# Optimization experiments

Hardware: AMD Instinct MI355X
Metric: run time of the kernel (lower is better)

Reference implementation:

```python
import jax, jax.numpy as jnp
import numpy as np

DIM = 512
NUM_HEADS = 8
HEAD_DIM = DIM // NUM_HEADS
SCALE = HEAD_DIM ** -0.5
B, T = 8, 1024


def setup_inputs() -> dict:
    key = jax.random.key(0)
    ks = jax.random.split(key, 6)
    x = jax.random.normal(ks[0], (B, T, DIM), dtype=jnp.float32)
    attn_mask = jax.random.randint(ks[1], (B, T, T), 0, 2) == 1  # bool [B,T,T]
    s = 1.0 / np.sqrt(DIM)
    qkv_w = jax.random.uniform(ks[2], (3 * DIM, DIM), jnp.float32, -s, s)
    qkv_b = jax.random.uniform(ks[3], (3 * DIM,), jnp.float32, -s, s)
    proj_w = jax.random.uniform(ks[4], (DIM, DIM), jnp.float32, -s, s)
    proj_b = jax.random.uniform(ks[5], (DIM,), jnp.float32, -s, s)
    return {"x": x, "attn_mask": attn_mask, "qkv_w": qkv_w, "qkv_b": qkv_b,
            "proj_w": proj_w, "proj_b": proj_b}


def reference(x, attn_mask, qkv_w, qkv_b, proj_w, proj_b):
    b, t, c = x.shape
    # QKV projection (torch Linear: x @ W.T + b), split into q,k,v heads
    qkv = x @ qkv_w.T + qkv_b                      # [b,t,3*c]
    qkv = qkv.reshape(b, t, 3, NUM_HEADS, HEAD_DIM)
    qkv = jnp.transpose(qkv, (2, 0, 3, 1, 4))      # [3,b,h,t,d]
    q, k, v = qkv[0], qkv[1], qkv[2]
    scores = jnp.einsum('bhqd,bhkd->bhqk', q, k) * SCALE  # [b,h,t,t]
    min_val = jnp.finfo(scores.dtype).min
    scores = jnp.where(attn_mask[:, None, :, :], min_val, scores)
    attn = jax.nn.softmax(scores, axis=-1)
    out = jnp.einsum('bhqk,bhkd->bhqd', attn, v)   # [b,h,t,d]
    out = jnp.transpose(out, (0, 2, 1, 3)).reshape(b, t, c)
    return out @ proj_w.T + proj_b
```

## Files before the change

kernel.cpp:

```cpp
#include <hip/hip_runtime.h>
#include <math.h>

#define DIM   512
#define NH    8
#define HD    64
#define BATCH 8
#define SEQ   1024
#define QSCALE 0.18033688011112042f

typedef unsigned short u16;
typedef unsigned int   u32;
typedef unsigned long long u64;
typedef __bf16 bf16x8 __attribute__((ext_vector_type(8)));
typedef float  f32x4  __attribute__((ext_vector_type(4)));

__device__ inline u16 f2bf(float f) {
  u32 u = __builtin_bit_cast(u32, f);
  return (u16)((u + 0x7fffu + ((u >> 16) & 1u)) >> 16);
}
__device__ inline float bf2f(u16 h) {
  return __builtin_bit_cast(float, (u32)h << 16);
}
__device__ inline u32 pk2(float a, float b) {
  return (u32)f2bf(a) | ((u32)f2bf(b) << 16);
}

__device__ inline void a16(const u16* g, u16* l) {
  __builtin_amdgcn_global_load_lds(
      (const __attribute__((address_space(1))) u32*)g,
      (__attribute__((address_space(3))) u32*)l, 16, 0, 0);
}


__device__ inline void decomp_body(const float* __restrict__ src, u16* ph,
                                   u16* pl, int t) {
  #pragma unroll
  for (int c = 0; c < 4; ++c) {
    const int cid = c * 256 + t;
    const int row = cid & 15, kc = cid >> 4;
    float f[8];
    *(float4*)&f[0] = *(const float4*)&src[row * DIM + kc * 8];
    *(float4*)&f[4] = *(const float4*)&src[row * DIM + kc * 8 + 4];
    u16 hv[8], lv[8];
    #pragma unroll
    for (int j = 0; j < 8; ++j) {
      hv[j] = f2bf(f[j]);
      lv[j] = f2bf(f[j] - bf2f(hv[j]));
    }
    *(uint4*)&ph[(size_t)cid * 8] = *(const uint4*)hv;
    *(uint4*)&pl[(size_t)cid * 8] = *(const uint4*)lv;
  }
}

__global__ __launch_bounds__(256) void prep(
    const int* __restrict__ mask, u64* __restrict__ bits,
    const float* __restrict__ x, u16* __restrict__ xhi, u16* __restrict__ xlo,
    const float* __restrict__ qkvw, u16* __restrict__ wqh, u16* __restrict__ wql,
    const float* __restrict__ projw, u16* __restrict__ wph, u16* __restrict__ wpl) {
  const int blk = blockIdx.x;
  const int t = threadIdx.x;
  if (blk < 32768) {
    const size_t gid = (size_t)blk * 256 + t;
    const int lane = t & 63;
    const size_t w = gid >> 6;
    const int v = mask[w * 64 + lane];
    const u64 b = __ballot(v != 0);
    if (lane == 0) {
      const int bb = (int)(w >> 14), q = (int)((w >> 4) & 1023),
                kt = (int)(w & 15);
      bits[(((size_t)(bb << 4 | kt)) << 10) | q] = b;
    }
  } else if (blk < 33280) {
    const int rg = blk - 32768;
    decomp_body(x + (size_t)rg * 16 * DIM, xhi + (size_t)rg * 8192,
                xlo + (size_t)rg * 8192, t);
  } else if (blk < 33376) {
    const int rg = blk - 33280;
    decomp_body(qkvw + (size_t)rg * 16 * DIM, wqh + (size_t)rg * 8192,
                wql + (size_t)rg * 8192, t);
  } else {
    const int rg = blk - 33376;
    decomp_body(projw + (size_t)rg * 16 * DIM, wph + (size_t)rg * 8192,
                wpl + (size_t)rg * 8192, t);
  }
}

template <bool QKV>
__global__ __launch_bounds__(256) void mfma_gemm(
    const u16* __restrict__ Agh, const u16* __restrict__ Agl,
    const u16* __restrict__ Bgh, const u16* __restrict__ Bgl,
    const float* __restrict__ bias, void* __restrict__ out0,
    u16* __restrict__ kfr, u16* __restrict__ vfr) {
  __shared__ u16 sAh[2][4096];
  __shared__ u16 sAl[2][4096];
  __shared__ u16 sBh[2][4096];
  __shared__ u16 sBl[2][4096];

  const int tid = threadIdx.x;
  const int lane = tid & 63;
  const int wv = tid >> 6;
  const int lk = lane & 15, lq = lane >> 4;
  const int m0 = blockIdx.x * 128, n0 = blockIdx.y * 128;
  const int wm = (wv & 1) * 4;
  const int wn = (wv >> 1) * 4;

  const u16* gAh = Agh + (size_t)(m0 >> 4) * 8192 + lane * 8;
  const u16* gAl = Agl + (size_t)(m0 >> 4) * 8192 + lane * 8;
  const u16* gBh = Bgh + (size_t)(n0 >> 4) * 8192 + lane * 8;
  const u16* gBl = Bgl + (size_t)(n0 >> 4) * 8192 + lane * 8;

  auto stage = [&](int bufi, int ki) {
    #pragma unroll
    for (int it = 0; it < 2; ++it) {
      const int t = it * 4 + wv;
      const size_t go = (size_t)t * 8192 + (size_t)ki * 512;
      const int lo_ = t * 512 + lane * 8;
      a16(gAh + go, &sAh[bufi][lo_]);
      a16(gAl + go, &sAl[bufi][lo_]);
      a16(gBh + go, &sBh[bufi][lo_]);
      a16(gBl + go, &sBl[bufi][lo_]);
    }
  };

  f32x4 acc[4][4];
  #pragma unroll
  for (int i = 0; i < 4; ++i)
    #pragma unroll
    for (int j = 0; j < 4; ++j) acc[i][j] = (f32x4){0.f, 0.f, 0.f, 0.f};

  stage(0, 0);
  __syncthreads();

  #pragma unroll 1
  for (int ki = 0; ki < 16; ++ki) {
    const int cur = ki & 1;
    bf16x8 ah[4], al[4], bh[4], bl[4];
    #pragma unroll
    for (int i = 0; i < 4; ++i) {
      ah[i] = *(const bf16x8*)&sAh[cur][(wm + i) * 512 + lane * 8];
      al[i] = *(const bf16x8*)&sAl[cur][(wm + i) * 512 + lane * 8];
      bh[i] = *(const bf16x8*)&sBh[cur][(wn + i) * 512 + lane * 8];
      bl[i] = *(const bf16x8*)&sBl[cur][(wn + i) * 512 + lane * 8];
    }
    if (ki < 15) stage(cur ^ 1, ki + 1);
    __builtin_amdgcn_sched_barrier(0);

    __builtin_amdgcn_s_setprio(1);
    #pragma unroll
    for (int i = 0; i < 4; ++i)
      #pragma unroll
      for (int j = 0; j < 4; ++j) {
        acc[i][j] = __builtin_amdgcn_mfma_f32_16x16x32_bf16(ah[i], bh[j], acc[i][j], 0, 0, 0);
        acc[i][j] = __builtin_amdgcn_mfma_f32_16x16x32_bf16(ah[i], bl[j], acc[i][j], 0, 0, 0);
        acc[i][j] = __builtin_amdgcn_mfma_f32_16x16x32_bf16(al[i], bh[j], acc[i][j], 0, 0, 0);
      }
    __builtin_amdgcn_s_setprio(0);

    __syncthreads();
  }

  #pragma unroll
  for (int j = 0; j < 4; ++j) {
    const int n = n0 + (wn + j) * 16 + lk;
    const float bv_ = bias[n];
    #pragma unroll
    for (int i = 0; i < 4; ++i) {
      const int mb = m0 + (wm + i) * 16 + lq * 4;
      if (QKV) {
        const int which = n >> 9, h = (n >> 6) & 7, d = n & 63;
        const int b = mb >> 10, tok0 = mb & 1023;
        const size_t hb = (size_t)((b << 3) + h) << 16;
        if (which == 2) {
          const size_t base = hb + ((size_t)(tok0 >> 6) << 12) +
                              ((size_t)((d >> 4) & 3) << 10) +
                              ((size_t)((tok0 >> 5) & 1) << 9) +
                              ((size_t)((d & 15) + (((tok0 >> 3) & 3) << 4)) << 3) +
                              (size_t)(tok0 & 7);
          uint2 o2;
          o2.x = pk2(acc[i][j][0] + bv_, acc[i][j][1] + bv_);
          o2.y = pk2(acc[i][j][2] + bv_, acc[i][j][3] + bv_);
          *(uint2*)&vfr[base] = o2;
        } else if (which == 1) {
          const size_t base = hb + ((size_t)(tok0 >> 4) << 10) +
                              ((size_t)(d >> 5) << 9) + (size_t)(d & 7) +
                              ((size_t)(((d >> 3) & 3) << 4) << 3);
          #pragma unroll
          for (int r = 0; r < 4; ++r)
            kfr[base + (((tok0 & 15) + r) << 3)] = f2bf(acc[i][j][r] + bv_);
        } else {
          u16* dst = (u16*)out0;
          #pragma unroll
          for (int r = 0; r < 4; ++r)
            dst[(((size_t)((b << 3) + h) << 10 | (tok0 + r)) << 6) + d] =
                f2bf((acc[i][j][r] + bv_) * QSCALE);
        }
      } else {
        #pragma unroll
        for (int r = 0; r < 4; ++r)
          ((float*)out0)[(size_t)(mb + r) * DIM + n] = acc[i][j][r] + bv_;
      }
    }
  }
}

__global__ __launch_bounds__(256) void attn_mfma(
    const u16* __restrict__ qg, const u16* __restrict__ kfr,
    const u16* __restrict__ vfr, const u64* __restrict__ bitsT,
    u16* __restrict__ ohi, u16* __restrict__ olo) {
  __shared__ u16 Kls[2][4096];
  __shared__ u16 Vls[2][4096];
  __shared__ u16 Ps[64 * 72];

  const int tid = threadIdx.x;
  const int lane = tid & 63;
  const int wv = tid >> 6;
  const int lk = lane & 15, lq = lane >> 4;
  const int bh = blockIdx.x;
  const int q0 = blockIdx.y * 64;
  const int bb = bh >> 3;
  const int q = q0 + wv * 16 + lk;

  const u16* qrow = qg + ((size_t)(bh << 10 | q) << 6);
  const bf16x8 bq0 = *(const bf16x8*)(qrow + lq * 8);
  const bf16x8 bq1 = *(const bf16x8*)(qrow + 32 + lq * 8);

  const u16* kh = kfr + ((size_t)bh << 16);
  const u16* vh = vfr + ((size_t)bh << 16);
  const u64* bitp = bitsT + ((size_t)bb << 14) + q;
  u16* pw = &Ps[(wv * 16 + lk) * 72];

  auto stage = [&](int bufi, int kt) {
    #pragma unroll
    for (int it = 0; it < 2; ++it) {
      const int c = it * 4 + wv;
      const int off = c * 512 + lane * 8;
      a16(kh + ((size_t)kt << 12) + off, &Kls[bufi][off]);
      a16(vh + ((size_t)kt << 12) + off, &Vls[bufi][off]);
    }
  };

  f32x4 o_[4];
  float l = 0.f;
  #pragma unroll
  for (int t = 0; t < 4; ++t) o_[t] = (f32x4){0.f, 0.f, 0.f, 0.f};

  stage(0, 0);
  __syncthreads();

  #pragma unroll 1
  for (int kt = 0; kt < 16; ++kt) {
    const int cur = kt & 1;
    const u64 wd = bitp[(size_t)kt << 10];

    bf16x8 ak0[4], ak1[4], vb0[4], vb1[4];
    #pragma unroll
    for (int t = 0; t < 4; ++t) {
      ak0[t] = *(const bf16x8*)&Kls[cur][t * 1024 + lane * 8];
      ak1[t] = *(const bf16x8*)&Kls[cur][t * 1024 + 512 + lane * 8];
      vb0[t] = *(const bf16x8*)&Vls[cur][t * 1024 + lane * 8];
      vb1[t] = *(const bf16x8*)&Vls[cur][t * 1024 + 512 + lane * 8];
    }
    if (kt < 15) stage(cur ^ 1, kt + 1);
    __builtin_amdgcn_sched_barrier(0);

    f32x4 st[4];
    const f32x4 z4 = (f32x4){0.f, 0.f, 0.f, 0.f};
    __builtin_amdgcn_s_setprio(1);
    #pragma unroll
    for (int t = 0; t < 4; ++t) {
      f32x4 a = __builtin_amdgcn_mfma_f32_16x16x32_bf16(ak0[t], bq0, z4, 0, 0, 0);
      st[t] = __builtin_amdgcn_mfma_f32_16x16x32_bf16(ak1[t], bq1, a, 0, 0, 0);
    }
    __builtin_amdgcn_s_setprio(0);

    const u32 w0 = (u32)wd, w1 = (u32)(wd >> 32);
    #pragma unroll
    for (int t = 0; t < 4; ++t) {
      const u32 w = (t < 2) ? w0 : w1;
      const int base = (t & 1) * 16 + lq * 4;
      float p[4];
      #pragma unroll
      for (int r = 0; r < 4; ++r) {
        const float sv = ((w >> (base + r)) & 1u) ? -INFINITY : st[t][r];
        p[r] = __builtin_amdgcn_exp2f(sv);
        l += p[r];
      }
      *(uint2*)(pw + t * 16 + lq * 4) = uint2{pk2(p[0], p[1]), pk2(p[2], p[3])};
    }

    const bf16x8 pa0 = *(const bf16x8*)(pw + lq * 8);
    const bf16x8 pa1 = *(const bf16x8*)(pw + 32 + lq * 8);
    __builtin_amdgcn_s_setprio(1);
    #pragma unroll
    for (int t = 0; t < 4; ++t) {
      o_[t] = __builtin_amdgcn_mfma_f32_16x16x32_bf16(pa0, vb0[t], o_[t], 0, 0, 0);
      o_[t] = __builtin_amdgcn_mfma_f32_16x16x32_bf16(pa1, vb1[t], o_[t], 0, 0, 0);
    }
    __builtin_amdgcn_s_setprio(0);

    __syncthreads();
  }

  l += __shfl_xor(l, 16);
  l += __shfl_xor(l, 32);

  const int h = bh & 7;
  #pragma unroll
  for (int r = 0; r < 4; ++r) {
    const float inv = 1.0f / __shfl(l, lq * 4 + r);
    const int tok = q0 + wv * 16 + lq * 4 + r;
    const int m = (bb << 10) | tok;
    const size_t rgo = (size_t)(m >> 4) * 8192 + (size_t)(m & 15) * 8;
    #pragma unroll
    for (int t = 0; t < 4; ++t) {
      const int d = t * 16 + lk;
      const int k = (h << 6) | d;
      const float v = o_[t][r] * inv;
      const u16 hv = f2bf(v);
      const size_t off = rgo + (size_t)(k >> 3) * 128 + (k & 7);
      ohi[off] = hv;
      olo[off] = f2bf(v - bf2f(hv));
    }
  }
}

extern "C" void kernel_launch(void* const* d_in, const int* in_sizes, int n_in,
                              void* d_out, int out_size, void* d_ws,
                              size_t ws_size, hipStream_t stream) {
  const float* x      = (const float*)d_in[0];
  const int*   mask   = (const int*)d_in[1];
  const float* qkv_w  = (const float*)d_in[2];
  const float* qkv_b  = (const float*)d_in[3];
  const float* proj_w = (const float*)d_in[4];
  const float* proj_b = (const float*)d_in[5];
  float* out = (float*)d_out;

  const size_t SZ = (size_t)BATCH * NH * SEQ * HD;
  u64* bits = (u64*)d_ws;
  u16* qb  = (u16*)(bits + 131072);
  u16* kfr = qb + SZ;
  u16* vfr = kfr + SZ;
  u16* xhi = vfr + SZ;
  u16* xlo = xhi + SZ;
  u16* ohi = xlo + SZ;
  u16* olo = ohi + SZ;
  u16* wqh = olo + SZ;
  u16* wql = wqh + 1536 * 512;
  u16* wph = wql + 1536 * 512;
  u16* wpl = wph + 512 * 512;

  prep<<<33408, 256, 0, stream>>>(mask, bits, x, xhi, xlo,
                                  qkv_w, wqh, wql, proj_w, wph, wpl);
  mfma_gemm<true><<<dim3(64, 12), 256, 0, stream>>>(
      xhi, xlo, wqh, wql, qkv_b, qb, kfr, vfr);
  attn_mfma<<<dim3(64, SEQ / 64), 256, 0, stream>>>(
      qb, kfr, vfr, bits, ohi, olo);
  mfma_gemm<false><<<dim3(64, 4), 256, 0, stream>>>(
      ohi, olo, wph, wpl, proj_b, out, nullptr, nullptr);
}
```

Before: 205.8 us.

## Load GEMM B operand directly from global and shrink proj GEMM M tile

The GEMM kernel no longer stages the weight (B) tiles through shared memory. Each wave reads its B fragments straight from global memory into registers, which halves LDS usage and allows launch_bounds occupancy of 3. The M tile becomes a template parameter, and the output projection uses a 64-row tile with twice as many blocks to fill more CUs. In exchange, B is fetched redundantly per wave from global/L2 with no prefetch ahead of use, so that load latency may be exposed.

```diff
diff --git a/kernel.cpp b/kernel.cpp
--- a/kernel.cpp
+++ b/kernel.cpp
@@ -85,69 +85,69 @@
   }
 }
 
-template <bool QKV>
-__global__ __launch_bounds__(256) void mfma_gemm(
+template <int MB, bool QKV>
+__global__ __launch_bounds__(256, 3) void mfma_gemm(
     const u16* __restrict__ Agh, const u16* __restrict__ Agl,
     const u16* __restrict__ Bgh, const u16* __restrict__ Bgl,
     const float* __restrict__ bias, void* __restrict__ out0,
     u16* __restrict__ kfr, u16* __restrict__ vfr) {
-  __shared__ u16 sAh[2][4096];
-  __shared__ u16 sAl[2][4096];
-  __shared__ u16 sBh[2][4096];
-  __shared__ u16 sBl[2][4096];
+  __shared__ u16 sAh[2][MB * 1024];
+  __shared__ u16 sAl[2][MB * 1024];
 
   const int tid = threadIdx.x;
   const int lane = tid & 63;
   const int wv = tid >> 6;
   const int lk = lane & 15, lq = lane >> 4;
-  const int m0 = blockIdx.x * 128, n0 = blockIdx.y * 128;
-  const int wm = (wv & 1) * 4;
+  const int m0 = blockIdx.x * (32 * MB), n0 = blockIdx.y * 128;
+  const int wm = (wv & 1) * MB;
   const int wn = (wv >> 1) * 4;
 
   const u16* gAh = Agh + (size_t)(m0 >> 4) * 8192 + lane * 8;
   const u16* gAl = Agl + (size_t)(m0 >> 4) * 8192 + lane * 8;
-  const u16* gBh = Bgh + (size_t)(n0 >> 4) * 8192 + lane * 8;
-  const u16* gBl = Bgl + (size_t)(n0 >> 4) * 8192 + lane * 8;
-
-  auto stage = [&](int bufi, int ki) {
-    #pragma unroll
-    for (int it = 0; it < 2; ++it) {
+  const u16* gB0h = Bgh + ((size_t)((n0 >> 4) + wn)) * 8192 + lane * 8;
+  const u16* gB0l = Bgl + ((size_t)((n0 >> 4) + wn)) * 8192 + lane * 8;
+
+  auto stageA = [&](int bufi, int ki) {
+    #pragma unroll
+    for (int it = 0; it < MB / 2; ++it) {
       const int t = it * 4 + wv;
       const size_t go = (size_t)t * 8192 + (size_t)ki * 512;
       const int lo_ = t * 512 + lane * 8;
       a16(gAh + go, &sAh[bufi][lo_]);
       a16(gAl + go, &sAl[bufi][lo_]);
-      a16(gBh + go, &sBh[bufi][lo_]);
-      a16(gBl + go, &sBl[bufi][lo_]);
     }
   };
 
-  f32x4 acc[4][4];
-  #pragma unroll
-  for (int i = 0; i < 4; ++i)
+  f32x4 acc[MB][4];
+  #pragma unroll
+  for (int i = 0; i < MB; ++i)
     #pragma unroll
     for (int j = 0; j < 4; ++j) acc[i][j] = (f32x4){0.f, 0.f, 0.f, 0.f};
 
-  stage(0, 0);
+  stageA(0, 0);
   __syncthreads();
 
   #pragma unroll 1
   for (int ki = 0; ki < 16; ++ki) {
     const int cur = ki & 1;
-    bf16x8 ah[4], al[4], bh[4], bl[4];
-    #pragma unroll
-    for (int i = 0; i < 4; ++i) {
+    bf16x8 bh[4], bl[4];
+    #pragma unroll
+    for (int j = 0; j < 4; ++j) {
+      bh[j] = *(const bf16x8*)(gB0h + (size_t)j * 8192 + (size_t)ki * 512);
+      bl[j] = *(const bf16x8*)(gB0l + (size_t)j * 8192 + (size_t)ki * 512);
+    }
+    bf16x8 ah[MB], al[MB];
+    #pragma unroll
+    for (int i = 0; i < MB; ++i) {
       ah[i] = *(const bf16x8*)&sAh[cur][(wm + i) * 512 + lane * 8];
       al[i] = *(const bf16x8*)&sAl[cur][(wm + i) * 512 + lane * 8];
-      bh[i] = *(const bf16x8*)&sBh[cur][(wn + i) * 512 + lane * 8];
-      bl[i] = *(const bf16x8*)&sBl[cur][(wn + i) * 512 + lane * 8];
-    }
-    if (ki < 15) stage(cur ^ 1, ki + 1);
+    }
+    if (ki < 15) stageA(cur ^ 1, ki + 1);
     __builtin_amdgcn_sched_barrier(0);
 
     __builtin_amdgcn_s_setprio(1);
     #pragma unroll
-    for (int i = 0; i < 4; ++i)
+    for (int i = 0; i < MB; ++i)
       #pragma unroll
       for (int j = 0; j < 4; ++j) {
         acc[i][j] = __builtin_amdgcn_mfma_f32_16x16x32_bf16(ah[i], bh[j], acc[i][j], 0, 0, 0);
@@ -164,7 +164,7 @@
     const int n = n0 + (wn + j) * 16 + lk;
     const float bv_ = bias[n];
     #pragma unroll
-    for (int i = 0; i < 4; ++i) {
+    for (int i = 0; i < MB; ++i) {
       const int mb = m0 + (wm + i) * 16 + lq * 4;
       if (QKV) {
         const int which = n >> 9, h = (n >> 6) & 7, d = n & 63;
@@ -351,10 +351,10 @@
 
   prep<<<33408, 256, 0, stream>>>(mask, bits, x, xhi, xlo,
                                   qkv_w, wqh, wql, proj_w, wph, wpl);
-  mfma_gemm<true><<<dim3(64, 12), 256, 0, stream>>>(
+  mfma_gemm<4, true><<<dim3(64, 12), 256, 0, stream>>>(
       xhi, xlo, wqh, wql, qkv_b, qb, kfr, vfr);
   attn_mfma<<<dim3(64, SEQ / 64), 256, 0, stream>>>(
       qb, kfr, vfr, bits, ohi, olo);
-  mfma_gemm<false><<<dim3(64, 4), 256, 0, stream>>>(
+  mfma_gemm<2, false><<<dim3(128, 4), 256, 0, stream>>>(
       ohi, olo, wph, wpl, proj_b, out, nullptr, nullptr);
 }
```

Result: no change. 207.4 us (+0.8%).
